# Optimization experiments

Hardware: AMD Instinct MI355X
Metric: run time of the kernel (lower is better)

## Reference

```python
import jax, jax.numpy as jnp
import numpy as np

N_EMBD = 1024
VOCAB = 64
B, T = 8, 4096


def setup_inputs() -> dict:
    key = jax.random.key(0)
    ks = jax.random.split(key, 6)
    x = jax.random.normal(ks[0], (B, T, N_EMBD), dtype=jnp.float32)
    idx = jax.random.randint(ks[1], (B, T), 0, VOCAB, dtype=jnp.int64)
    emb_weight = jax.random.normal(ks[2], (VOCAB, N_EMBD), dtype=jnp.float32)
    head_weight = jax.random.normal(ks[3], (VOCAB, N_EMBD), dtype=jnp.float32)
    gate = jax.random.normal(ks[4], (1, 1, N_EMBD), dtype=jnp.float32) * 0.01
    soft_gate = jax.random.normal(ks[5], (1, 1, N_EMBD), dtype=jnp.float32) * 0.01
    return {"x": x, "idx": idx, "emb_weight": emb_weight,
            "head_weight": head_weight, "gate": gate, "soft_gate": soft_gate}


def reference(x, idx, emb_weight, head_weight, gate, soft_gate):
    # --- idx-gated codebook blend (idx from previous step's argmax, clamped >= 0) ---
    idx_c = jnp.clip(idx, 0, None)
    emb = emb_weight[idx_c]                                  # [B,T,D]
    g = jax.nn.sigmoid(x * gate).mean(axis=-1, keepdims=True)  # [B,T,1]
    x = x * (1.0 - g) + emb * g
    # (tmix/cmix are external and treated as identity here)
    # --- small-vocab head + softmax-weighted codebook lookup ---
    logits = jnp.einsum('btd,vd->btv', x, head_weight)        # [B,T,64]
    soft_prob = jax.nn.softmax(logits, axis=-1)
    soft_emb = jnp.einsum('btv,vd->btd', soft_prob, emb_weight)
    sg = jax.nn.sigmoid(x * soft_gate).mean(axis=-1, keepdims=True)
    x = x * (1.0 - sg) + soft_emb * sg
    # --- argmax indexing for next step ---
    new_idx = jnp.argmax(logits, axis=-1)                     # [B,T]
    return x, new_idx
```

## Files before the change

### kernel.cpp

```cpp
#include <hip/hip_runtime.h>
#include <hip/hip_bf16.h>


#define DIMS 1024
#define VOCAB 64
#define NTOK 32768
#define TTILE 16
#define TPB 512
#define IDX_OFF (NTOK * DIMS)

typedef __attribute__((ext_vector_type(8))) short short8;
typedef __attribute__((ext_vector_type(4))) float f32x4;

__device__ __forceinline__ float sigm(float z) {
    return 1.f / (1.f + __expf(-z));
}
__device__ __forceinline__ unsigned short f2bf(float f) {
    __hip_bfloat16 h = __float2bfloat16(f);
    return *reinterpret_cast<unsigned short*>(&h);
}

__global__ void prep_weights(const float* __restrict__ head,
                             const float* __restrict__ emb,
                             __hip_bfloat16* __restrict__ headB,
                             __hip_bfloat16* __restrict__ embT) {
    int t = blockIdx.x * 256 + threadIdx.x;
    int v = t >> 10, d = t & 1023;
    headB[t] = __float2bfloat16(head[t]);
    embT[d * VOCAB + v] = __float2bfloat16(emb[v * DIMS + d]);
}

__global__ __launch_bounds__(TPB, 6) void fused_block(
    const float* __restrict__ x,
    const int* __restrict__ idx,
    const float* __restrict__ emb,
    const float* __restrict__ gate,
    const float* __restrict__ sgate,
    const float* __restrict__ headF,
    const __hip_bfloat16* __restrict__ headB,
    const __hip_bfloat16* __restrict__ embT,
    float* __restrict__ out)
{
    __shared__ __align__(16) __hip_bfloat16 sX1b[TTILE][1032];
    __shared__ __align__(16) float          sLogP[2][TTILE][68];
    __shared__ __align__(16) __hip_bfloat16 sP[TTILE][72];
    __shared__ float sSg[TTILE];

    const int tid  = threadIdx.x;
    const int tk   = tid >> 5;
    const int l32  = tid & 31;
    const long t0  = (long)blockIdx.x * TTILE;
    const long tok = t0 + tk;

    float4 xv[8];
    float gsum = 0.f;
    const float4* xrow = (const float4*)(x + tok * DIMS);
    const float4* grow = (const float4*)gate;
    #pragma unroll
    for (int c = 0; c < 8; c++) {
        int f = l32 + c * 32;
        float4 v = xrow[f];
        float4 gv = grow[f];
        xv[c] = v;
        gsum += sigm(v.x * gv.x) + sigm(v.y * gv.y)
              + sigm(v.z * gv.z) + sigm(v.w * gv.w);
    }
    gsum += __shfl_xor(gsum, 1); gsum += __shfl_xor(gsum, 2);
    gsum += __shfl_xor(gsum, 4); gsum += __shfl_xor(gsum, 8);
    gsum += __shfl_xor(gsum, 16);
    const float g = gsum * (1.f / 1024.f);

    int ic = idx[tok]; if (ic < 0) ic = 0;
    const float4* erow = (const float4*)(emb + (long)ic * DIMS);
    const float4* srow = (const float4*)sgate;
    float ssum = 0.f;
    #pragma unroll
    for (int c = 0; c < 8; c++) {
        int f = l32 + c * 32;
        float4 ev = erow[f];
        float4 sv = srow[f];
        float4 a;
        a.x = xv[c].x * (1.f - g) + ev.x * g;
        a.y = xv[c].y * (1.f - g) + ev.y * g;
        a.z = xv[c].z * (1.f - g) + ev.z * g;
        a.w = xv[c].w * (1.f - g) + ev.w * g;
        xv[c] = a;
        ssum += sigm(a.x * sv.x) + sigm(a.y * sv.y)
              + sigm(a.z * sv.z) + sigm(a.w * sv.w);
        ushort4 pk;
        pk.x = f2bf(a.x); pk.y = f2bf(a.y); pk.z = f2bf(a.z); pk.w = f2bf(a.w);
        *(ushort4*)&sX1b[tk][f * 4] = pk;
    }
    ssum += __shfl_xor(ssum, 1); ssum += __shfl_xor(ssum, 2);
    ssum += __shfl_xor(ssum, 4); ssum += __shfl_xor(ssum, 8);
    ssum += __shfl_xor(ssum, 16);
    if (l32 == 0) sSg[tk] = ssum * (1.f / 1024.f);
    __syncthreads();

    const int w    = tid >> 6;
    const int lane = tid & 63;
    const int quad = lane >> 4, l16 = lane & 15;
    const int nt   = w & 3;
    const int kh   = w >> 2;
    {
        f32x4 acc = {0.f, 0.f, 0.f, 0.f};
        const __hip_bfloat16* hrow = headB + (long)(nt * 16 + l16) * DIMS + kh * 512 + quad * 8;
        #pragma unroll 4
        for (int k0 = 0; k0 < 512; k0 += 32) {
            short8 a = *(const short8*)&sX1b[l16][kh * 512 + k0 + quad * 8];
            short8 b = *(const short8*)(hrow + k0);
            acc = __builtin_amdgcn_mfma_f32_16x16x32_bf16(a, b, acc, 0, 0, 0);
        }
        #pragma unroll
        for (int i = 0; i < 4; i++)
            sLogP[kh][quad * 4 + i][nt * 16 + l16] = acc[i];
    }
    __syncthreads();

    int cA[4], cB[4];
    #pragma unroll
    for (int it = 0; it < 2; it++) {
        int m = 2 * w + it;
        float l0 = sLogP[0][m][lane] + sLogP[1][m][lane];
        float mx = l0;
        mx = fmaxf(mx, __shfl_xor(mx, 1));  mx = fmaxf(mx, __shfl_xor(mx, 2));
        mx = fmaxf(mx, __shfl_xor(mx, 4));  mx = fmaxf(mx, __shfl_xor(mx, 8));
        mx = fmaxf(mx, __shfl_xor(mx, 16)); mx = fmaxf(mx, __shfl_xor(mx, 32));
        float e = __expf(l0 - mx);
        float s = e;
        s += __shfl_xor(s, 1);  s += __shfl_xor(s, 2);  s += __shfl_xor(s, 4);
        s += __shfl_xor(s, 8);  s += __shfl_xor(s, 16); s += __shfl_xor(s, 32);
        sP[m][lane] = __float2bfloat16(e / s);
        float l = l0;
        #pragma unroll
        for (int j = 0; j < 4; j++) {
            float mj = l;
            mj = fmaxf(mj, __shfl_xor(mj, 1));  mj = fmaxf(mj, __shfl_xor(mj, 2));
            mj = fmaxf(mj, __shfl_xor(mj, 4));  mj = fmaxf(mj, __shfl_xor(mj, 8));
            mj = fmaxf(mj, __shfl_xor(mj, 16)); mj = fmaxf(mj, __shfl_xor(mj, 32));
            int cj = __ffsll(__ballot(l == mj)) - 1;
            if (lane == cj) l = -3.4e38f;
            if (it == 0) cA[j] = cj; else cB[j] = cj;
        }
    }

    {
        const int h = (lane >> 5) & 1;
        int rows[4];
        #pragma unroll
        for (int j = 0; j < 4; j++) rows[j] = h ? cB[j] : cA[j];
        float tot[4];
        #pragma unroll
        for (int j = 0; j < 4; j++) {
            const float4* hr = (const float4*)(headF + (long)rows[j] * DIMS);
            float p = 0.f;
            #pragma unroll
            for (int c = 0; c < 8; c++) {
                float4 hv = hr[l32 + c * 32];
                p = fmaf(xv[c].x, hv.x, p); p = fmaf(xv[c].y, hv.y, p);
                p = fmaf(xv[c].z, hv.z, p); p = fmaf(xv[c].w, hv.w, p);
            }
            p += __shfl_xor(p, 1); p += __shfl_xor(p, 2);
            p += __shfl_xor(p, 4); p += __shfl_xor(p, 8);
            p += __shfl_xor(p, 16);
            tot[j] = p;
        }
        if (l32 == 0) {
            float bv = tot[0]; int bi = rows[0];
            #pragma unroll
            for (int j = 1; j < 4; j++) {
                if (tot[j] > bv || (tot[j] == bv && rows[j] < bi)) {
                    bv = tot[j]; bi = rows[j];
                }
            }
            out[IDX_OFF + tok] = (float)bi;
        }
    }
    __syncthreads();

    #pragma unroll 1
    for (int i = 0; i < 8; i++) {
        int n0 = (i * 8 + w) * 16;
        f32x4 acc = {0.f, 0.f, 0.f, 0.f};
        #pragma unroll
        for (int k0 = 0; k0 < VOCAB; k0 += 32) {
            short8 a = *(const short8*)&sP[l16][k0 + quad * 8];
            short8 b = *(const short8*)(embT + (long)(n0 + l16) * VOCAB + k0 + quad * 8);
            acc = __builtin_amdgcn_mfma_f32_16x16x32_bf16(a, b, acc, 0, 0, 0);
        }
        #pragma unroll
        for (int r = 0; r < 4; r++) {
            int m = quad * 4 + r;
            int n = n0 + l16;
            float sg = sSg[m];
            float x1f = __bfloat162float(sX1b[m][n]);
            out[(t0 + m) * (long)DIMS + n] = x1f * (1.f - sg) + acc[r] * sg;
        }
    }
}

extern "C" void kernel_launch(void* const* d_in, const int* in_sizes, int n_in,
                              void* d_out, int out_size, void* d_ws, size_t ws_size,
                              hipStream_t stream) {
    const float* xp    = (const float*)d_in[0];
    const int*   idxp  = (const int*)d_in[1];
    const float* embp  = (const float*)d_in[2];
    const float* headp = (const float*)d_in[3];
    const float* gp    = (const float*)d_in[4];
    const float* sgp   = (const float*)d_in[5];
    float*       outp  = (float*)d_out;

    __hip_bfloat16* headB = (__hip_bfloat16*)d_ws;
    __hip_bfloat16* embT  = (__hip_bfloat16*)((char*)d_ws + 131072);

    prep_weights<<<dim3(256), dim3(256), 0, stream>>>(headp, embp, headB, embT);
    fused_block<<<dim3(NTOK / TTILE), dim3(TPB), 0, stream>>>(
        xp, idxp, embp, gp, sgp, headp, headB, embT, outp);
}
```

Before: 309.0 us.

## Restructure head GEMM, margin-based argmax candidates, and coalesced output epilogue

The head logits GEMM now runs on four waves over the full K with two accumulators, so the split-K reduction goes away. The argmax refinement is no longer a fixed top-4. It checks every logit within a fixed margin of the max, recomputing it as an fp32 dot product. The soft-embedding MFMA now swaps its operands and writes bf16 results back into shared memory. A final pass then writes whole output rows as coalesced float4 using the fp32 x held in registers, replacing the scattered strided stores. Launch bounds occupancy is raised from 6 to 8. The risks are that the candidate loop length now depends on the data, that occupancy 8 may cause register spills, and that the softmax-embedding term is rounded to bf16.

Measured after the change: 373.1 us. 20.7% more time.

```diff
diff --git a/kernel.cpp b/kernel.cpp
--- a/kernel.cpp
+++ b/kernel.cpp
@@ -8,6 +8,7 @@
 #define TTILE 16
 #define TPB 512
 #define IDX_OFF (NTOK * DIMS)
+#define CAND_DELTA 2.5f
 
 typedef __attribute__((ext_vector_type(8))) short short8;
 typedef __attribute__((ext_vector_type(4))) float f32x4;
@@ -18,6 +19,10 @@
 __device__ __forceinline__ unsigned short f2bf(float f) {
     __hip_bfloat16 h = __float2bfloat16(f);
     return *reinterpret_cast<unsigned short*>(&h);
+}
+__device__ __forceinline__ float bf2f(unsigned short u) {
+    __hip_bfloat16 h = *reinterpret_cast<__hip_bfloat16*>(&u);
+    return __bfloat162float(h);
 }
 
 __global__ void prep_weights(const float* __restrict__ head,
@@ -30,7 +35,7 @@
     embT[d * VOCAB + v] = __float2bfloat16(emb[v * DIMS + d]);
 }
 
-__global__ __launch_bounds__(TPB, 6) void fused_block(
+__global__ __launch_bounds__(TPB, 8) void fused_block(
     const float* __restrict__ x,
     const int* __restrict__ idx,
     const float* __restrict__ emb,
@@ -42,7 +47,7 @@
     float* __restrict__ out)
 {
     __shared__ __align__(16) __hip_bfloat16 sX1b[TTILE][1032];
-    __shared__ __align__(16) float          sLogP[2][TTILE][68];
+    __shared__ __align__(16) float          sLogP[TTILE][66];
     __shared__ __align__(16) __hip_bfloat16 sP[TTILE][72];
     __shared__ float sSg[TTILE];
 
@@ -100,59 +105,55 @@
     const int w    = tid >> 6;
     const int lane = tid & 63;
     const int quad = lane >> 4, l16 = lane & 15;
-    const int nt   = w & 3;
-    const int kh   = w >> 2;
-    {
-        f32x4 acc = {0.f, 0.f, 0.f, 0.f};
-        const __hip_bfloat16* hrow = headB + (long)(nt * 16 + l16) * DIMS + kh * 512 + quad * 8;
-        #pragma unroll 4
-        for (int k0 = 0; k0 < 512; k0 += 32) {
-            short8 a = *(const short8*)&sX1b[l16][kh * 512 + k0 + quad * 8];
-            short8 b = *(const short8*)(hrow + k0);
-            acc = __builtin_amdgcn_mfma_f32_16x16x32_bf16(a, b, acc, 0, 0, 0);
+    if (w < 4) {
+        f32x4 acc0 = {0.f, 0.f, 0.f, 0.f};
+        f32x4 acc1 = {0.f, 0.f, 0.f, 0.f};
+        const __hip_bfloat16* hrow = headB + (long)(w * 16 + l16) * DIMS + quad * 8;
+        #pragma unroll 2
+        for (int k0 = 0; k0 < 1024; k0 += 64) {
+            short8 a0 = *(const short8*)&sX1b[l16][k0 + quad * 8];
+            short8 b0 = *(const short8*)(hrow + k0);
+            acc0 = __builtin_amdgcn_mfma_f32_16x16x32_bf16(a0, b0, acc0, 0, 0, 0);
+            short8 a1 = *(const short8*)&sX1b[l16][k0 + 32 + quad * 8];
+            short8 b1 = *(const short8*)(hrow + k0 + 32);
+            acc1 = __builtin_amdgcn_mfma_f32_16x16x32_bf16(a1, b1, acc1, 0, 0, 0);
         }
         #pragma unroll
         for (int i = 0; i < 4; i++)
-            sLogP[kh][quad * 4 + i][nt * 16 + l16] = acc[i];
-    }
-    __syncthreads();
-
-    int cA[4], cB[4];
-    #pragma unroll
-    for (int it = 0; it < 2; it++) {
-        int m = 2 * w + it;
-        float l0 = sLogP[0][m][lane] + sLogP[1][m][lane];
-        float mx = l0;
-        mx = fmaxf(mx, __shfl_xor(mx, 1));  mx = fmaxf(mx, __shfl_xor(mx, 2));
-        mx = fmaxf(mx, __shfl_xor(mx, 4));  mx = fmaxf(mx, __shfl_xor(mx, 8));
-        mx = fmaxf(mx, __shfl_xor(mx, 16)); mx = fmaxf(mx, __shfl_xor(mx, 32));
-        float e = __expf(l0 - mx);
-        float s = e;
-        s += __shfl_xor(s, 1);  s += __shfl_xor(s, 2);  s += __shfl_xor(s, 4);
-        s += __shfl_xor(s, 8);  s += __shfl_xor(s, 16); s += __shfl_xor(s, 32);
-        sP[m][lane] = __float2bfloat16(e / s);
-        float l = l0;
-        #pragma unroll
-        for (int j = 0; j < 4; j++) {
-            float mj = l;
-            mj = fmaxf(mj, __shfl_xor(mj, 1));  mj = fmaxf(mj, __shfl_xor(mj, 2));
-            mj = fmaxf(mj, __shfl_xor(mj, 4));  mj = fmaxf(mj, __shfl_xor(mj, 8));
-            mj = fmaxf(mj, __shfl_xor(mj, 16)); mj = fmaxf(mj, __shfl_xor(mj, 32));
-            int cj = __ffsll(__ballot(l == mj)) - 1;
-            if (lane == cj) l = -3.4e38f;
-            if (it == 0) cA[j] = cj; else cB[j] = cj;
-        }
-    }
-
-    {
-        const int h = (lane >> 5) & 1;
-        int rows[4];
-        #pragma unroll
-        for (int j = 0; j < 4; j++) rows[j] = h ? cB[j] : cA[j];
-        float tot[4];
-        #pragma unroll
-        for (int j = 0; j < 4; j++) {
-            const float4* hr = (const float4*)(headF + (long)rows[j] * DIMS);
+            sLogP[quad * 4 + i][w * 16 + l16] = acc0[i] + acc1[i];
+    }
+    __syncthreads();
+
+    unsigned long long candA, candB;
+    {
+        float lA = sLogP[2 * w][lane];
+        float lB = sLogP[2 * w + 1][lane];
+        float mA = lA, mB = lB;
+        #pragma unroll
+        for (int k = 1; k < 64; k <<= 1) {
+            mA = fmaxf(mA, __shfl_xor(mA, k));
+            mB = fmaxf(mB, __shfl_xor(mB, k));
+        }
+        float eA = __expf(lA - mA), eB = __expf(lB - mB);
+        float sA = eA, sB = eB;
+        #pragma unroll
+        for (int k = 1; k < 64; k <<= 1) {
+            sA += __shfl_xor(sA, k);
+            sB += __shfl_xor(sB, k);
+        }
+        sP[2 * w][lane]     = __float2bfloat16(eA / sA);
+        sP[2 * w + 1][lane] = __float2bfloat16(eB / sB);
+        candA = __ballot(lA >= mA - CAND_DELTA);
+        candB = __ballot(lB >= mB - CAND_DELTA);
+    }
+
+    {
+        unsigned long long cm = ((lane >> 5) & 1) ? candB : candA;
+        float bv = -3.4e38f; int bi = 0;
+        while (cm) {
+            int v = __ffsll(cm) - 1;
+            cm &= cm - 1;
+            const float4* hr = (const float4*)(headF + (long)v * DIMS);
             float p = 0.f;
             #pragma unroll
             for (int c = 0; c < 8; c++) {
@@ -163,38 +164,43 @@
             p += __shfl_xor(p, 1); p += __shfl_xor(p, 2);
             p += __shfl_xor(p, 4); p += __shfl_xor(p, 8);
             p += __shfl_xor(p, 16);
-            tot[j] = p;
-        }
-        if (l32 == 0) {
-            float bv = tot[0]; int bi = rows[0];
-            #pragma unroll
-            for (int j = 1; j < 4; j++) {
-                if (tot[j] > bv || (tot[j] == bv && rows[j] < bi)) {
-                    bv = tot[j]; bi = rows[j];
-                }
-            }
-            out[IDX_OFF + tok] = (float)bi;
-        }
-    }
-    __syncthreads();
-
-    #pragma unroll 1
-    for (int i = 0; i < 8; i++) {
-        int n0 = (i * 8 + w) * 16;
-        f32x4 acc = {0.f, 0.f, 0.f, 0.f};
-        #pragma unroll
-        for (int k0 = 0; k0 < VOCAB; k0 += 32) {
-            short8 a = *(const short8*)&sP[l16][k0 + quad * 8];
-            short8 b = *(const short8*)(embT + (long)(n0 + l16) * VOCAB + k0 + quad * 8);
-            acc = __builtin_amdgcn_mfma_f32_16x16x32_bf16(a, b, acc, 0, 0, 0);
-        }
-        #pragma unroll
-        for (int r = 0; r < 4; r++) {
-            int m = quad * 4 + r;
-            int n = n0 + l16;
-            float sg = sSg[m];
-            float x1f = __bfloat162float(sX1b[m][n]);
-            out[(t0 + m) * (long)DIMS + n] = x1f * (1.f - sg) + acc[r] * sg;
+            if (p > bv) { bv = p; bi = v; }
+        }
+        if (l32 == 0) out[IDX_OFF + tok] = (float)bi;
+    }
+    __syncthreads();
+
+    {
+        short8 pb0 = *(const short8*)&sP[l16][quad * 8];
+        short8 pb1 = *(const short8*)&sP[l16][32 + quad * 8];
+        #pragma unroll 2
+        for (int i = 0; i < 8; i++) {
+            int n0 = (i * 8 + w) * 16;
+            const __hip_bfloat16* er = embT + (long)(n0 + l16) * VOCAB + quad * 8;
+            f32x4 acc = {0.f, 0.f, 0.f, 0.f};
+            acc = __builtin_amdgcn_mfma_f32_16x16x32_bf16(*(const short8*)er, pb0, acc, 0, 0, 0);
+            acc = __builtin_amdgcn_mfma_f32_16x16x32_bf16(*(const short8*)(er + 32), pb1, acc, 0, 0, 0);
+            ushort4 pk;
+            pk.x = f2bf(acc[0]); pk.y = f2bf(acc[1]);
+            pk.z = f2bf(acc[2]); pk.w = f2bf(acc[3]);
+            *(ushort4*)&sX1b[l16][n0 + quad * 4] = pk;
+        }
+    }
+    __syncthreads();
+
+    {
+        const float sg = sSg[tk];
+        float4* orow = (float4*)(out + tok * DIMS);
+        #pragma unroll
+        for (int c = 0; c < 8; c++) {
+            int f = l32 + c * 32;
+            ushort4 se = *(const ushort4*)&sX1b[tk][f * 4];
+            float4 o;
+            o.x = xv[c].x * (1.f - sg) + bf2f(se.x) * sg;
+            o.y = xv[c].y * (1.f - sg) + bf2f(se.y) * sg;
+            o.z = xv[c].z * (1.f - sg) + bf2f(se.z) * sg;
+            o.w = xv[c].w * (1.f - sg) + bf2f(se.w) * sg;
+            orow[f] = o;
         }
     }
 }
```
